# Kernel tuning notes

Hardware: AMD Instinct MI355X
Metric: run time of the kernel (lower is better)

## Reference

```python
import jax, jax.numpy as jnp
import numpy as np

EMBED_DIM = 256
B, H, S = 8, 20, 1024


def setup_inputs() -> dict:
    key = jax.random.key(0)
    ks = jax.random.split(key, 10)
    E = EMBED_DIM
    d2, d4 = 2 * E, 4 * E

    def lin(kw, kb, out_dim, in_dim):
        bound = 1.0 / np.sqrt(in_dim)
        w = jax.random.uniform(kw, (out_dim, in_dim), minval=-bound, maxval=bound, dtype=jnp.float32)
        b = jax.random.uniform(kb, (out_dim,), minval=-bound, maxval=bound, dtype=jnp.float32)
        return w, b

    wc_w, wc_b = lin(ks[0], ks[1], d2, d2)
    wh_w, wh_b = lin(ks[2], ks[3], d2, d2)
    qt_w, qt_b = lin(ks[4], ks[5], 1, d2)
    wf_w, wf_b = lin(ks[6], ks[7], E, d4)

    hist = jax.random.normal(ks[8], (B, H, S, d2), dtype=jnp.float32)
    cur = jax.random.normal(ks[9], (B, S, d2), dtype=jnp.float32)
    return {
        "wca_history_embeddings": hist,
        "wca_current_embeddings": cur,
        "wc_w": wc_w, "wc_b": wc_b,
        "wh_w": wh_w, "wh_b": wh_b,
        "qt_w": qt_w, "qt_b": qt_b,
        "wf_w": wf_w, "wf_b": wf_b,
    }


def reference(wca_history_embeddings, wca_current_embeddings,
              wc_w, wc_b, wh_w, wh_b, qt_w, qt_b, wf_w, wf_b):
    # hist: [B, H, S, 2E]; cur: [B, S, 2E]
    c_proj = jnp.einsum('bsd,ed->bse', wca_current_embeddings, wc_w) + wc_b   # [B,S,2E]
    h_proj = jnp.einsum('bhsd,ed->bhse', wca_history_embeddings, wh_w) + wh_b  # [B,H,S,2E]
    gate = jax.nn.sigmoid(c_proj[:, None, :, :] + h_proj)                      # [B,H,S,2E]
    # alpha[b,h,s] = qt(gate) -- raw scores, NO softmax (matches original)
    alpha = jnp.einsum('bhse,e->bhs', gate, qt_w[0]) + qt_b[0]                 # [B,H,S]
    # weighted neighbor sum over history dim
    summed = jnp.einsum('bhs,bhsd->bsd', alpha, wca_history_embeddings)        # [B,S,2E]
    fused = jnp.concatenate([wca_current_embeddings, summed], axis=-1)         # [B,S,4E]
    final = jnp.einsum('bsd,ed->bse', fused, wf_w) + wf_b                      # [B,S,E]
    return final
```

## Files before the change

### kernel.cpp

```cpp
#include <hip/hip_runtime.h>
#include <hip/hip_bf16.h>
#include <stdint.h>

static constexpr int Bn = 8, Hn = 20, Sn = 1024, En = 256, D2 = 512, D4 = 1024;
static constexpr int Mall = Bn * Hn * Sn;
static constexpr int BS   = Bn * Sn;

typedef __attribute__((ext_vector_type(8))) short bf16x8;
typedef __attribute__((ext_vector_type(4))) float f32x4;

__device__ __forceinline__ unsigned short f2bf(float f) {
  unsigned int u = __float_as_uint(f);
  u += 0x7FFFu + ((u >> 16) & 1u);
  return (unsigned short)(u >> 16);
}
__device__ __forceinline__ float bf2f(unsigned short u) {
  return __uint_as_float(((unsigned int)u) << 16);
}
__device__ __forceinline__ float sigmoid_fast(float x) {
  return __builtin_amdgcn_rcpf(1.0f + __expf(-x));
}
__device__ __forceinline__ unsigned int packbf_trunc(float a, float b) {
  return __builtin_amdgcn_perm(__float_as_uint(b), __float_as_uint(a),
                               0x07060302u);
}
__device__ __forceinline__ unsigned int packbf_rne(float a, float b) {
  return ((unsigned int)f2bf(b) << 16) | (unsigned int)f2bf(a);
}
__device__ __forceinline__ uint4 pack8_trunc(float4 f0, float4 f1) {
  uint4 p;
  p.x = packbf_trunc(f0.x, f0.y);
  p.y = packbf_trunc(f0.z, f0.w);
  p.z = packbf_trunc(f1.x, f1.y);
  p.w = packbf_trunc(f1.z, f1.w);
  return p;
}
__device__ __forceinline__ bf16x8 pack2(float4 f0, float4 f1) {
  union { uint4 u; bf16x8 b; } c;
  c.u = pack8_trunc(f0, f1);
  return c.b;
}

typedef const __attribute__((address_space(1))) void gv_t;
typedef __attribute__((address_space(3))) void lv_t;
__device__ __forceinline__ void gload_lds16(const void* g, void* l) {
  __builtin_amdgcn_global_load_lds((gv_t*)g, (lv_t*)l, 16, 0, 0);
}

__global__ __launch_bounds__(256) void k_convert_weights(
    const float* __restrict__ wc, const float* __restrict__ wh,
    const float* __restrict__ wf,
    unsigned short* __restrict__ wcb, unsigned short* __restrict__ whb,
    unsigned short* __restrict__ wfb) {
  int idx4 = blockIdx.x * 256 + threadIdx.x;
  int a = idx4 >> 16;
  int r = idx4 & 65535;
  const float* s = (a == 0) ? wc : (a == 1) ? wh : wf;
  unsigned short* d = (a == 0) ? wcb : (a == 1) ? whb : wfb;
  float4 v = reinterpret_cast<const float4*>(s)[r];
  ushort4 o;
  o.x = f2bf(v.x); o.y = f2bf(v.y); o.z = f2bf(v.z); o.w = f2bf(v.w);
  reinterpret_cast<ushort4*>(d)[r] = o;
}

template <int MODE>
__global__ __launch_bounds__(256) void k_gemm_bt(
    const float* __restrict__ A,
    const unsigned short* __restrict__ Bw,
    const float* __restrict__ bias,
    const unsigned short* __restrict__ cproj,
    const float* __restrict__ qtw,
    const float* __restrict__ qtb,
    unsigned short* __restrict__ cproj_out,
    float* __restrict__ alpha_out) {
  __shared__ __align__(16) unsigned char ldsA[128 * 128];
  __shared__ __align__(16) unsigned char ldsB[128 * 128];

  const int tid = threadIdx.x;
  const int lane = tid & 63, wave = tid >> 6;
  const int lrow = lane & 15, lk = lane >> 4;
  const int row0 = blockIdx.x * 128;
  const f32x4 zero4 = {0.f, 0.f, 0.f, 0.f};

  float asum[2][4];
  if (MODE == 1) {
#pragma unroll
    for (int rf = 0; rf < 2; ++rf)
#pragma unroll
      for (int r = 0; r < 4; ++r) asum[rf][r] = 0.f;
  }

  const int nc_begin = (MODE == 0) ? blockIdx.y : 0;
  const int nc_end   = (MODE == 0) ? (int)blockIdx.y + 1 : 4;

  for (int nc = nc_begin; nc < nc_end; ++nc) {
    f32x4 acc[2][8];
#pragma unroll
    for (int rf = 0; rf < 2; ++rf)
#pragma unroll
      for (int cf = 0; cf < 8; ++cf) acc[rf][cf] = zero4;

    for (int kt = 0; kt < 8; ++kt) {
      __syncthreads();
#pragma unroll
      for (int slot = 0; slot < 4; ++slot) {
        int idx = (slot * 256 + tid) * 8;
        int row = idx >> 6, k = idx & 63;
        const float* src = A + (size_t)(row0 + row) * 512 + kt * 64 + k;
        float4 f0 = *reinterpret_cast<const float4*>(src);
        float4 f1 = *reinterpret_cast<const float4*>(src + 4);
        uint4 p = pack8_trunc(f0, f1);
        int off = row * 128 + ((k * 2) ^ ((row & 7) << 4));
        *reinterpret_cast<uint4*>(ldsA + off) = p;
      }
#pragma unroll
      for (int c = 0; c < 4; ++c) {
        int ci = c * 256 + tid;
        int n = ci >> 3, kc = (ci & 7) * 8;
        const unsigned short* src =
            Bw + (size_t)(nc * 128 + n) * 512 + kt * 64 + kc;
        uint4 p = *reinterpret_cast<const uint4*>(src);
        int off = n * 128 + ((kc * 2) ^ ((n & 7) << 4));
        *reinterpret_cast<uint4*>(ldsB + off) = p;
      }
      __syncthreads();
#pragma unroll
      for (int ks = 0; ks < 2; ++ks) {
        int kbyte = ks * 64 + lk * 16;
        bf16x8 af[2];
#pragma unroll
        for (int rf = 0; rf < 2; ++rf) {
          int ar = wave * 32 + rf * 16 + lrow;
          af[rf] = *reinterpret_cast<const bf16x8*>(
              ldsA + ar * 128 + (kbyte ^ ((ar & 7) << 4)));
        }
#pragma unroll
        for (int cf = 0; cf < 8; ++cf) {
          int br = cf * 16 + lrow;
          bf16x8 bf = *reinterpret_cast<const bf16x8*>(
              ldsB + br * 128 + (kbyte ^ ((br & 7) << 4)));
#pragma unroll
          for (int rf = 0; rf < 2; ++rf)
            acc[rf][cf] = __builtin_amdgcn_mfma_f32_16x16x32_bf16(
                af[rf], bf, acc[rf][cf], 0, 0, 0);
        }
      }
    }

    if (MODE == 0) {
#pragma unroll
      for (int cf = 0; cf < 8; ++cf) {
        int e = nc * 128 + cf * 16 + lrow;
        float bse = bias[e];
#pragma unroll
        for (int rf = 0; rf < 2; ++rf)
#pragma unroll
          for (int r = 0; r < 4; ++r) {
            int row = row0 + wave * 32 + rf * 16 + lk * 4 + r;
            cproj_out[(size_t)row * 512 + e] = f2bf(acc[rf][cf][r] + bse);
          }
      }
    } else {
#pragma unroll
      for (int cf = 0; cf < 8; ++cf) {
        int e = nc * 128 + cf * 16 + lrow;
        float whb = bias[e];
        float qw = qtw[e];
#pragma unroll
        for (int rf = 0; rf < 2; ++rf)
#pragma unroll
          for (int r = 0; r < 4; ++r) {
            int row = row0 + wave * 32 + rf * 16 + lk * 4 + r;
            int bsrow = ((row / (Hn * Sn)) << 10) | (row & 1023);
            float cp = bf2f(cproj[(size_t)bsrow * 512 + e]);
            float g = sigmoid_fast(acc[rf][cf][r] + whb + cp);
            asum[rf][r] = fmaf(g, qw, asum[rf][r]);
          }
      }
    }
  }

  if (MODE == 1) {
#pragma unroll
    for (int off = 1; off < 16; off <<= 1) {
#pragma unroll
      for (int rf = 0; rf < 2; ++rf)
#pragma unroll
        for (int r = 0; r < 4; ++r)
          asum[rf][r] += __shfl_xor(asum[rf][r], off, 64);
    }
    if (lrow == 0) {
      float qb = qtb[0];
#pragma unroll
      for (int rf = 0; rf < 2; ++rf)
#pragma unroll
        for (int r = 0; r < 4; ++r) {
          int row = row0 + wave * 32 + rf * 16 + lk * 4 + r;
          alpha_out[row] = asum[rf][r] + qb;
        }
    }
  }
}

__global__ __launch_bounds__(256, 2) void k_alpha(
    const float* __restrict__ A,
    const unsigned short* __restrict__ Bw,
    const float* __restrict__ bias,
    const unsigned short* __restrict__ cproj,
    const float* __restrict__ qtw,
    const float* __restrict__ qtb,
    float* __restrict__ alpha) {
  __shared__ __align__(16) unsigned char ldsA[16384];
  __shared__ __align__(16) unsigned char ldsB[65536];

  const int tid = threadIdx.x;
  const int lane = tid & 63, wave = tid >> 6;
  const int lrow = lane & 15, lk = lane >> 4;
  const int wr = wave >> 1, wc = wave & 1;
  const int p = blockIdx.x;
  const int xb = (p & 7) * 320 + (p >> 3);
  const int row0 = xb * 64;
  const f32x4 zero4 = {0.f, 0.f, 0.f, 0.f};

  const int arow = tid >> 4;
  const int aslot = (tid & 15) ^ (arow & 15);
  const float* gA0 = A + (size_t)(row0 + arow) * 512 + aslot * 4;
  const int brow = tid >> 3;
  const int bslot = (tid & 7) ^ (brow & 7);
  const unsigned short* gB0 = Bw + (size_t)brow * 512 + bslot * 8;
  char* lA = (char*)ldsA + wave * 1024;
  char* lB = (char*)ldsB + wave * 1024;

  f32x4 acc[2][16];
#pragma unroll
  for (int m = 0; m < 2; ++m)
#pragma unroll
    for (int n = 0; n < 16; ++n) acc[m][n] = zero4;

  for (int kt = 0; kt < 8; ++kt) {
    __syncthreads();
#pragma unroll
    for (int j = 0; j < 4; ++j)
      gload_lds16(gA0 + j * 8192 + kt * 64, lA + j * 4096);
#pragma unroll
    for (int j = 0; j < 16; ++j)
      gload_lds16(gB0 + j * 16384 + kt * 64, lB + j * 4096);
    __syncthreads();
#pragma unroll
    for (int ks = 0; ks < 2; ++ks) {
      bf16x8 af[2];
#pragma unroll
      for (int m = 0; m < 2; ++m) {
        int r = wr * 32 + m * 16 + lrow;
        int q0 = (ks * 8 + lk * 2) ^ (r & 15);
        int q1 = (ks * 8 + lk * 2 + 1) ^ (r & 15);
        float4 d0 = *reinterpret_cast<const float4*>(ldsA + r * 256 + q0 * 16);
        float4 d1 = *reinterpret_cast<const float4*>(ldsA + r * 256 + q1 * 16);
        af[m] = pack2(d0, d1);
      }
#pragma unroll
      for (int n = 0; n < 16; ++n) {
        int r = wc * 256 + n * 16 + lrow;
        int slot = (ks * 4 + lk) ^ (r & 7);
        bf16x8 bv =
            *reinterpret_cast<const bf16x8*>(ldsB + r * 128 + slot * 16);
#pragma unroll
        for (int m = 0; m < 2; ++m)
          acc[m][n] = __builtin_amdgcn_mfma_f32_16x16x32_bf16(af[m], bv,
                                                              acc[m][n], 0, 0,
                                                              0);
      }
    }
  }

  float asum[2][4];
#pragma unroll
  for (int m = 0; m < 2; ++m)
#pragma unroll
    for (int r = 0; r < 4; ++r) asum[m][r] = 0.f;

  const size_t cpbase = ((size_t)(row0 / (Hn * Sn)) * 1024 + (row0 & 1023)) * 512;
#pragma unroll
  for (int n = 0; n < 16; ++n) {
    int e = wc * 256 + n * 16 + lrow;
    float whb = bias[e];
    float qw = qtw[e];
#pragma unroll
    for (int m = 0; m < 2; ++m)
#pragma unroll
      for (int r = 0; r < 4; ++r) {
        int t = wr * 32 + m * 16 + lk * 4 + r;
        float cp = bf2f(cproj[cpbase + (size_t)t * 512 + e]);
        float g = sigmoid_fast(acc[m][n][r] + whb + cp);
        asum[m][r] = fmaf(g, qw, asum[m][r]);
      }
  }
#pragma unroll
  for (int off = 1; off < 16; off <<= 1)
#pragma unroll
    for (int m = 0; m < 2; ++m)
#pragma unroll
      for (int r = 0; r < 4; ++r)
        asum[m][r] += __shfl_xor(asum[m][r], off, 64);

  __syncthreads();
  float* red = reinterpret_cast<float*>(ldsA);
  if (lrow == 0) {
#pragma unroll
    for (int m = 0; m < 2; ++m)
#pragma unroll
      for (int r = 0; r < 4; ++r)
        red[wc * 64 + wr * 32 + m * 16 + lk * 4 + r] = asum[m][r];
  }
  __syncthreads();
  if (tid < 64) alpha[row0 + tid] = red[tid] + red[64 + tid] + qtb[0];
}

__global__ __launch_bounds__(256) void k_summed(
    const float* __restrict__ hist, const float* __restrict__ alpha,
    unsigned short* __restrict__ summed) {
  int idx = blockIdx.x * 256 + threadIdx.x;
  int bs = idx >> 7, c4 = idx & 127;
  int b = bs >> 10, s = bs & 1023;
  const float4* hp = reinterpret_cast<const float4*>(hist);
  float4 acc = make_float4(0.f, 0.f, 0.f, 0.f);
#pragma unroll
  for (int h = 0; h < Hn; ++h) {
    int bh = b * Hn + h;
    float a = alpha[(bh << 10) + s];
    float4 v = hp[(size_t)(bh * 1024 + s) * 128 + c4];
    acc.x = fmaf(a, v.x, acc.x);
    acc.y = fmaf(a, v.y, acc.y);
    acc.z = fmaf(a, v.z, acc.z);
    acc.w = fmaf(a, v.w, acc.w);
  }
  ushort4 o;
  o.x = f2bf(acc.x); o.y = f2bf(acc.y); o.z = f2bf(acc.z); o.w = f2bf(acc.w);
  reinterpret_cast<ushort4*>(summed)[idx] = o;
}

__global__ __launch_bounds__(256) void k_final(
    const float* __restrict__ cur,
    const unsigned short* __restrict__ summed,
    const unsigned short* __restrict__ wfb16,
    const float* __restrict__ wf_bias,
    float* __restrict__ out) {
  __shared__ __align__(16) unsigned char ldsA[64 * 128];
  __shared__ __align__(16) unsigned char ldsB[128 * 128];
  const int tid = threadIdx.x;
  const int lane = tid & 63, wave = tid >> 6;
  const int lrow = lane & 15, lk = lane >> 4;
  const int row0 = blockIdx.x * 64;
  const int n0 = blockIdx.y * 128;
  const f32x4 zero4 = {0.f, 0.f, 0.f, 0.f};

  f32x4 acc[8];
#pragma unroll
  for (int cf = 0; cf < 8; ++cf) acc[cf] = zero4;

  for (int kt = 0; kt < 16; ++kt) {
    __syncthreads();
#pragma unroll
    for (int slot = 0; slot < 2; ++slot) {
      int idx = (slot * 256 + tid) * 8;
      int row = idx >> 6, k = idx & 63;
      int gcol = kt * 64 + k;
      uint4 p;
      if (kt < 8) {
        const float* src = cur + (size_t)(row0 + row) * 512 + gcol;
        float4 f0 = *reinterpret_cast<const float4*>(src);
        float4 f1 = *reinterpret_cast<const float4*>(src + 4);
        p = pack8_trunc(f0, f1);
      } else {
        p = *reinterpret_cast<const uint4*>(
            summed + (size_t)(row0 + row) * 512 + gcol - 512);
      }
      int off = row * 128 + ((k * 2) ^ ((row & 7) << 4));
      *reinterpret_cast<uint4*>(ldsA + off) = p;
    }
#pragma unroll
    for (int c = 0; c < 4; ++c) {
      int ci = c * 256 + tid;
      int n = ci >> 3, kc = (ci & 7) * 8;
      uint4 p = *reinterpret_cast<const uint4*>(
          wfb16 + (size_t)(n0 + n) * 1024 + kt * 64 + kc);
      int off = n * 128 + ((kc * 2) ^ ((n & 7) << 4));
      *reinterpret_cast<uint4*>(ldsB + off) = p;
    }
    __syncthreads();
#pragma unroll
    for (int ks = 0; ks < 2; ++ks) {
      int kbyte = ks * 64 + lk * 16;
      int ar = wave * 16 + lrow;
      bf16x8 a = *reinterpret_cast<const bf16x8*>(
          ldsA + ar * 128 + (kbyte ^ ((ar & 7) << 4)));
#pragma unroll
      for (int cf = 0; cf < 8; ++cf) {
        int br = cf * 16 + lrow;
        bf16x8 b = *reinterpret_cast<const bf16x8*>(
            ldsB + br * 128 + (kbyte ^ ((br & 7) << 4)));
        acc[cf] = __builtin_amdgcn_mfma_f32_16x16x32_bf16(a, b, acc[cf], 0, 0, 0);
      }
    }
  }
#pragma unroll
  for (int cf = 0; cf < 8; ++cf) {
    int col = n0 + cf * 16 + lrow;
    float bse = wf_bias[col];
#pragma unroll
    for (int r = 0; r < 4; ++r) {
      int row = row0 + wave * 16 + lk * 4 + r;
      out[(size_t)row * 256 + col] = acc[cf][r] + bse;
    }
  }
}

extern "C" void kernel_launch(void* const* d_in, const int* in_sizes, int n_in,
                              void* d_out, int out_size, void* d_ws,
                              size_t ws_size, hipStream_t stream) {
  (void)in_sizes; (void)n_in; (void)out_size;
  const float* hist = (const float*)d_in[0];
  const float* cur  = (const float*)d_in[1];
  const float* wc_w = (const float*)d_in[2];
  const float* wc_b = (const float*)d_in[3];
  const float* wh_w = (const float*)d_in[4];
  const float* wh_b = (const float*)d_in[5];
  const float* qt_w = (const float*)d_in[6];
  const float* qt_b = (const float*)d_in[7];
  const float* wf_w = (const float*)d_in[8];
  const float* wf_b = (const float*)d_in[9];
  float* out = (float*)d_out;
  char* ws = (char*)d_ws;

  unsigned short* wcb    = (unsigned short*)(ws);
  unsigned short* whb    = (unsigned short*)(ws + 524288);
  unsigned short* wfb    = (unsigned short*)(ws + 1048576);
  unsigned short* cproj  = (unsigned short*)(ws + 1572864);
  float*          alpha  = (float*)(ws + 9961472);
  unsigned short* summed = (unsigned short*)(ws + 10616832);
  const size_t NEED = 19005440;

  k_convert_weights<<<dim3(768), dim3(256), 0, stream>>>(wc_w, wh_w, wf_w, wcb,
                                                         whb, wfb);
  k_gemm_bt<0><<<dim3(BS / 128, 4), dim3(256), 0, stream>>>(
      cur, wcb, wc_b, nullptr, nullptr, nullptr, cproj, nullptr);
  if (ws_size >= NEED) {
    k_alpha<<<dim3(Mall / 64), dim3(256), 0, stream>>>(hist, whb, wh_b, cproj,
                                                       qt_w, qt_b, alpha);
  } else {
    k_gemm_bt<1><<<dim3(Mall / 128, 1), dim3(256), 0, stream>>>(
        hist, whb, wh_b, cproj, qt_w, qt_b, nullptr, alpha);
  }
  k_summed<<<dim3(4096), dim3(256), 0, stream>>>(hist, alpha, summed);
  k_final<<<dim3(BS / 64, 2), dim3(256), 0, stream>>>(cur, summed, wfb, wf_b,
                                                      out);
}
```

Before: 242.7 us.

## Prefetch A tile via registers, store bf16 in LDS, split waves along N

The alpha GEMM kernel now loads the next fp32 A tile into registers during the current MFMA phase, converts it to bf16 once, and writes it to a swizzled LDS buffer. Previously the fp32 tile was copied straight into LDS and repacked by every wave. Each wave now covers all 64 rows and a 128-column slice instead of a 2x2 row/column split, and the final reduction sums four partials instead of two. This is meant to overlap global loads with compute and cut repeated conversion work. The cost is more registers for the prefetch buffers, and the B loads are still not double-buffered.

```diff
diff --git a/kernel.cpp b/kernel.cpp
--- a/kernel.cpp
+++ b/kernel.cpp
@@ -34,11 +34,6 @@
   p.z = packbf_trunc(f1.x, f1.y);
   p.w = packbf_trunc(f1.z, f1.w);
   return p;
-}
-__device__ __forceinline__ bf16x8 pack2(float4 f0, float4 f1) {
-  union { uint4 u; bf16x8 b; } c;
-  c.u = pack8_trunc(f0, f1);
-  return c.b;
 }
 
 typedef const __attribute__((address_space(1))) void gv_t;
@@ -210,86 +205,113 @@
     const float* __restrict__ qtw,
     const float* __restrict__ qtb,
     float* __restrict__ alpha) {
-  __shared__ __align__(16) unsigned char ldsA[16384];
+  __shared__ __align__(16) unsigned char ldsA[8192];
   __shared__ __align__(16) unsigned char ldsB[65536];
 
   const int tid = threadIdx.x;
   const int lane = tid & 63, wave = tid >> 6;
   const int lrow = lane & 15, lk = lane >> 4;
-  const int wr = wave >> 1, wc = wave & 1;
+  const int wc = wave;
   const int p = blockIdx.x;
   const int xb = (p & 7) * 320 + (p >> 3);
   const int row0 = xb * 64;
   const f32x4 zero4 = {0.f, 0.f, 0.f, 0.f};
 
-  const int arow = tid >> 4;
-  const int aslot = (tid & 15) ^ (arow & 15);
-  const float* gA0 = A + (size_t)(row0 + arow) * 512 + aslot * 4;
   const int brow = tid >> 3;
   const int bslot = (tid & 7) ^ (brow & 7);
   const unsigned short* gB0 = Bw + (size_t)brow * 512 + bslot * 8;
-  char* lA = (char*)ldsA + wave * 1024;
   char* lB = (char*)ldsB + wave * 1024;
-
-  f32x4 acc[2][16];
-#pragma unroll
-  for (int m = 0; m < 2; ++m)
-#pragma unroll
-    for (int n = 0; n < 16; ++n) acc[m][n] = zero4;
-
-  for (int kt = 0; kt < 8; ++kt) {
-    __syncthreads();
-#pragma unroll
-    for (int j = 0; j < 4; ++j)
-      gload_lds16(gA0 + j * 8192 + kt * 64, lA + j * 4096);
+  auto issueB = [&](int kt) {
 #pragma unroll
     for (int j = 0; j < 16; ++j)
       gload_lds16(gB0 + j * 16384 + kt * 64, lB + j * 4096);
-    __syncthreads();
+  };
+
+  float4 pa[4];
+  auto loadA = [&](int kt) {
+#pragma unroll
+    for (int j = 0; j < 2; ++j) {
+      int f = j * 256 + tid;
+      int row = f >> 3, g = f & 7;
+      const float* src = A + (size_t)(row0 + row) * 512 + kt * 64 + g * 8;
+      pa[j * 2]     = *reinterpret_cast<const float4*>(src);
+      pa[j * 2 + 1] = *reinterpret_cast<const float4*>(src + 4);
+    }
+  };
+  auto writeA = [&]() {
+#pragma unroll
+    for (int j = 0; j < 2; ++j) {
+      int f = j * 256 + tid;
+      int row = f >> 3, g = f & 7;
+      int off = row * 128 + ((g ^ (row & 7)) << 4);
+      *reinterpret_cast<uint4*>(ldsA + off) =
+          pack8_trunc(pa[j * 2], pa[j * 2 + 1]);
+    }
+  };
+
+  f32x4 acc[4][8];
+#pragma unroll
+  for (int m = 0; m < 4; ++m)
+#pragma unroll
+    for (int n = 0; n < 8; ++n) acc[m][n] = zero4;
+
+  loadA(0);
+  issueB(0);
+  writeA();
+  __syncthreads();
+
+  for (int kt = 0; kt < 8; ++kt) {
+    if (kt < 7) {
+      loadA(kt + 1);
+      __builtin_amdgcn_sched_barrier(0);
+    }
 #pragma unroll
     for (int ks = 0; ks < 2; ++ks) {
-      bf16x8 af[2];
-#pragma unroll
-      for (int m = 0; m < 2; ++m) {
-        int r = wr * 32 + m * 16 + lrow;
-        int q0 = (ks * 8 + lk * 2) ^ (r & 15);
-        int q1 = (ks * 8 + lk * 2 + 1) ^ (r & 15);
-        float4 d0 = *reinterpret_cast<const float4*>(ldsA + r * 256 + q0 * 16);
-        float4 d1 = *reinterpret_cast<const float4*>(ldsA + r * 256 + q1 * 16);
-        af[m] = pack2(d0, d1);
-      }
-#pragma unroll
-      for (int n = 0; n < 16; ++n) {
-        int r = wc * 256 + n * 16 + lrow;
+      bf16x8 af[4];
+#pragma unroll
+      for (int m = 0; m < 4; ++m) {
+        int r = m * 16 + lrow;
         int slot = (ks * 4 + lk) ^ (r & 7);
+        af[m] = *reinterpret_cast<const bf16x8*>(ldsA + r * 128 + slot * 16);
+      }
+#pragma unroll
+      for (int n = 0; n < 8; ++n) {
+        int rb = wc * 128 + n * 16 + lrow;
+        int slot = (ks * 4 + lk) ^ (rb & 7);
         bf16x8 bv =
-            *reinterpret_cast<const bf16x8*>(ldsB + r * 128 + slot * 16);
-#pragma unroll
-        for (int m = 0; m < 2; ++m)
+            *reinterpret_cast<const bf16x8*>(ldsB + rb * 128 + slot * 16);
+#pragma unroll
+        for (int m = 0; m < 4; ++m)
           acc[m][n] = __builtin_amdgcn_mfma_f32_16x16x32_bf16(af[m], bv,
                                                               acc[m][n], 0, 0,
                                                               0);
       }
     }
-  }
-
-  float asum[2][4];
-#pragma unroll
-  for (int m = 0; m < 2; ++m)
+    __syncthreads();
+    if (kt < 7) {
+      issueB(kt + 1);
+      writeA();
+      __syncthreads();
+    }
+  }
+
+  float asum[4][4];
+#pragma unroll
+  for (int m = 0; m < 4; ++m)
 #pragma unroll
     for (int r = 0; r < 4; ++r) asum[m][r] = 0.f;
 
   const size_t cpbase = ((size_t)(row0 / (Hn * Sn)) * 1024 + (row0 & 1023)) * 512;
 #pragma unroll
-  for (int n = 0; n < 16; ++n) {
-    int e = wc * 256 + n * 16 + lrow;
+  for (int n = 0; n < 8; ++n) {
+    int e = wc * 128 + n * 16 + lrow;
     float whb = bias[e];
     float qw = qtw[e];
 #pragma unroll
-    for (int m = 0; m < 2; ++m)
+    for (int m = 0; m < 4; ++m)
 #pragma unroll
       for (int r = 0; r < 4; ++r) {
-        int t = wr * 32 + m * 16 + lk * 4 + r;
+        int t = m * 16 + lk * 4 + r;
         float cp = bf2f(cproj[cpbase + (size_t)t * 512 + e]);
         float g = sigmoid_fast(acc[m][n][r] + whb + cp);
         asum[m][r] = fmaf(g, qw, asum[m][r]);
@@ -298,7 +320,7 @@
 #pragma unroll
   for (int off = 1; off < 16; off <<= 1)
 #pragma unroll
-    for (int m = 0; m < 2; ++m)
+    for (int m = 0; m < 4; ++m)
 #pragma unroll
       for (int r = 0; r < 4; ++r)
         asum[m][r] += __shfl_xor(asum[m][r], off, 64);
@@ -307,13 +329,15 @@
   float* red = reinterpret_cast<float*>(ldsA);
   if (lrow == 0) {
 #pragma unroll
-    for (int m = 0; m < 2; ++m)
+    for (int m = 0; m < 4; ++m)
 #pragma unroll
       for (int r = 0; r < 4; ++r)
-        red[wc * 64 + wr * 32 + m * 16 + lk * 4 + r] = asum[m][r];
+        red[wc * 64 + m * 16 + lk * 4 + r] = asum[m][r];
   }
   __syncthreads();
-  if (tid < 64) alpha[row0 + tid] = red[tid] + red[64 + tid] + qtb[0];
+  if (tid < 64)
+    alpha[row0 + tid] =
+        red[tid] + red[64 + tid] + red[128 + tid] + red[192 + tid] + qtb[0];
 }
 
 __global__ __launch_bounds__(256) void k_summed(
```

Measured after the change: 262.2 us. 1.08x slower.
